# Kernel tuning notes

Measured on AMD Instinct MI355X. Metric: run time of the kernel, lower is better.

The kernel has to match this reference:

```python
import jax, jax.numpy as jnp
import numpy as np

D_MODEL = 1024
N_HEADS = 16
D_K = D_MODEL // N_HEADS
SIGMA = 1.0
NUM_ITERS = 3
PAD_POS = 10000.0


def setup_inputs() -> dict:
    rng = jax.random.key(0)
    ks = jax.random.split(rng, 16)
    B, Lq, Lk = 8, 512, 512
    s = 1.0 / np.sqrt(D_MODEL).astype(np.float32)
    return {
        "query": jax.random.normal(ks[0], (B, Lq, D_MODEL), jnp.float32),
        "key": jax.random.normal(ks[1], (B, Lk, D_MODEL), jnp.float32),
        "value": jax.random.normal(ks[2], (B, Lk, D_MODEL), jnp.float32),
        "query_lengths": jax.random.randint(ks[3], (B,), 2, Lq),
        "key_lengths": jax.random.randint(ks[4], (B,), 2, Lk),
        "Wq": jax.random.normal(ks[5], (D_MODEL, D_MODEL), jnp.float32) * s,
        "bq": jnp.zeros((D_MODEL,), jnp.float32),
        "Wk": jax.random.normal(ks[6], (D_MODEL, D_MODEL), jnp.float32) * s,
        "bk": jnp.zeros((D_MODEL,), jnp.float32),
        "Wv": jax.random.normal(ks[7], (D_MODEL, D_MODEL), jnp.float32) * s,
        "bv": jnp.zeros((D_MODEL,), jnp.float32),
        "Wo": jax.random.normal(ks[8], (D_MODEL, D_MODEL), jnp.float32) * s,
        "bo": jnp.zeros((D_MODEL,), jnp.float32),
        "pos_scale": jnp.ones((1,), jnp.float32),
        "pos_bias": jnp.zeros((1,), jnp.float32),
    }


def _init_positions(lengths, max_len, scale, bias):
    # vectorized tcr_pep init: linspace(-L/2, L/2, L) per row, pad -> 10000
    j = jnp.arange(max_len, dtype=jnp.float32)[None, :]          # [1, L]
    L = lengths.astype(jnp.float32)[:, None]                      # [B, 1]
    step = jnp.where(L > 1.0, L / (L - 1.0), 0.0)                 # linspace step
    pos = (-L / 2.0 + j * step) * scale + bias
    pad = jnp.arange(max_len)[None, :] >= lengths[:, None]
    return jnp.where(pad, PAD_POS, pos)


def _distance_attention(qp, kp):
    d2 = (qp[:, :, None] - kp[:, None, :]) ** 2                   # [B, Lq, Lk]
    attn = jnp.exp(-d2 / (2.0 * SIGMA * SIGMA))
    masked = (qp[:, :, None] >= 1000.0) | (kp[:, None, :] >= 1000.0)
    return jnp.where(masked, 0.0, attn)


def _update_positions(qp, kp, attn):
    qn = attn / jnp.clip(attn.sum(-1, keepdims=True), 1e-9)
    qp_new = jnp.einsum('bqk,bk->bq', qn, kp)
    at = attn.transpose(0, 2, 1)
    kn = at / jnp.clip(at.sum(-1, keepdims=True), 1e-9)
    kp_new = jnp.einsum('bkq,bq->bk', kn, qp)
    qp_new = jnp.where(qp >= 1000.0, PAD_POS, qp_new)
    kp_new = jnp.where(kp >= 1000.0, PAD_POS, kp_new)
    return qp_new, kp_new


def reference(query, key, value, query_lengths, key_lengths,
              Wq, bq, Wk, bk, Wv, bv, Wo, bo, pos_scale, pos_bias):
    B, Lq, _ = query.shape
    Lk = key.shape[1]

    def split_heads(x):
        return x.reshape(B, -1, N_HEADS, D_K).transpose(0, 2, 1, 3)  # [B,H,L,Dk]

    q = split_heads(query @ Wq.T + bq)
    k = split_heads(key @ Wk.T + bk)
    v = split_heads(value @ Wv.T + bv)

    qp = _init_positions(query_lengths, Lq, pos_scale, pos_bias)  # [B, Lq]
    kp = _init_positions(key_lengths, Lk, pos_scale, pos_bias)    # [B, Lk]

    scores = jnp.einsum('bhqd,bhkd->bhqk', q, k) / jnp.sqrt(jnp.float32(D_K))
    attn = jax.nn.softmax(scores, axis=-1)                        # [B,H,Lq,Lk]

    for _ in range(NUM_ITERS):
        da = _distance_attention(qp, kp)                          # [B,Lq,Lk]
        comb = attn * da[:, None, :, :]
        comb = comb / jnp.clip(comb.sum(-1, keepdims=True), 1e-9)
        qp, kp = _update_positions(qp, kp, da)
        attn = comb

    ctx = jnp.einsum('bhqk,bhkd->bhqd', attn, v)
    ctx = ctx.transpose(0, 2, 1, 3).reshape(B, Lq, D_MODEL)
    out = ctx @ Wo.T + bo
    return out, attn.mean(axis=1)
```

## Files before the change

kernel.cpp:

```cpp
#include <hip/hip_runtime.h>
#include <math.h>

#define B_  8
#define LQ  512
#define LK  512
#define DM  1024
#define NH  16
#define DK  64
constexpr float PADP = 10000.0f;

typedef short s16x8 __attribute__((ext_vector_type(8)));
typedef float f32x4 __attribute__((ext_vector_type(4)));

__device__ inline unsigned short f2b1(float f) {
    unsigned u = __float_as_uint(f);
    unsigned r = (u + 0x7fffu + ((u >> 16) & 1u)) >> 16;
    return (unsigned short)r;
}
__device__ inline float b2f1(unsigned short h) {
    return __uint_as_float(((unsigned)h) << 16);
}

__global__ __launch_bounds__(256) void f2b_all_kernel(
    const float* __restrict__ query, const float* __restrict__ key,
    const float* __restrict__ value,
    const float* __restrict__ Wq, const float* __restrict__ Wk,
    const float* __restrict__ Wv, const float* __restrict__ Wo,
    unsigned short* __restrict__ xq, unsigned short* __restrict__ xk,
    unsigned short* __restrict__ xv,
    unsigned short* __restrict__ wqb, unsigned short* __restrict__ wkb,
    unsigned short* __restrict__ wvb, unsigned short* __restrict__ wob)
{
    const int s = blockIdx.y;
    const float* src;
    unsigned short* dst;
    if (s < 4)       { src = query + ((size_t)s << 20);       dst = xq + ((size_t)s << 20); }
    else if (s < 8)  { src = key   + ((size_t)(s - 4) << 20); dst = xk + ((size_t)(s - 4) << 20); }
    else if (s < 12) { src = value + ((size_t)(s - 8) << 20); dst = xv + ((size_t)(s - 8) << 20); }
    else {
        const int w = s - 12;
        src = (w == 0) ? Wq : (w == 1) ? Wk : (w == 2) ? Wv : Wo;
        dst = (w == 0) ? wqb : (w == 1) ? wkb : (w == 2) ? wvb : wob;
    }
    const int i = blockIdx.x * 256 + threadIdx.x;
    const float4 v = *(const float4*)&src[(size_t)i * 4];
    ushort4 o;
    o.x = f2b1(v.x); o.y = f2b1(v.y); o.z = f2b1(v.z); o.w = f2b1(v.w);
    *(ushort4*)&dst[(size_t)i * 4] = o;
}

template <int PHASE>
__global__ __launch_bounds__(512) void daRow_kernel(
    const int* __restrict__ qlen, const int* __restrict__ klen,
    const float* __restrict__ pscale, const float* __restrict__ pbias,
    float* __restrict__ posQ,
    const float* __restrict__ posKin, float* __restrict__ posKout,
    const float* __restrict__ rsIn, const float* __restrict__ rdIn,
    const float* __restrict__ colSIn, const float* __restrict__ colDIn,
    float* __restrict__ rsOut, float* __restrict__ rdOut,
    float* __restrict__ colSOut, float* __restrict__ colDOut,
    unsigned short* __restrict__ Dplane)
{
    constexpr int NCH = 16, QC = LQ / NCH;
    __shared__ float kpl[LK];
    __shared__ float csp[8][LK], cdp[8][LK];
    const int chunk = blockIdx.x, b = blockIdx.y;
    const int t = threadIdx.x, w = t >> 6, lane = t & 63;

    float scale = 0.0f, bias = 0.0f;
    if (PHASE == 0) { scale = pscale[0]; bias = pbias[0]; }

    if (PHASE == 0) {
        const int kl = klen[b];
        const float Lf = (float)kl;
        const float step = (Lf > 1.0f) ? Lf / (Lf - 1.0f) : 0.0f;
        const float pos = (-Lf * 0.5f + (float)t * step) * scale + bias;
        const float kv = (t >= kl) ? PADP : pos;
        kpl[t] = kv;
        if (chunk == 0) posKout[b * LK + t] = kv;
    } else {
        float colsum = 0.0f, coldot = 0.0f;
#pragma unroll
        for (int c = 0; c < NCH; ++c) {
            colsum += colSIn[((size_t)b * NCH + c) * LK + t];
            coldot += colDIn[((size_t)b * NCH + c) * LK + t];
        }
        const float prev = posKin[b * LK + t];
        const float kv = (prev >= 1000.0f) ? PADP : coldot / fmaxf(colsum, 1e-9f);
        kpl[t] = kv;
        if (PHASE == 1 && chunk == 0) posKout[b * LK + t] = kv;
    }
    __syncthreads();

    float cs[8] = {0,0,0,0,0,0,0,0}, cd[8] = {0,0,0,0,0,0,0,0};
    unsigned short* Dbb = Dplane + (size_t)b * LQ * LK;

    for (int qi = chunk * QC + w; qi < chunk * QC + QC; qi += 8) {
        float qpv;
        if (PHASE == 0) {
            const int ql = qlen[b];
            const float Lf = (float)ql;
            const float step = (Lf > 1.0f) ? Lf / (Lf - 1.0f) : 0.0f;
            qpv = (qi >= ql) ? PADP : (-Lf * 0.5f + (float)qi * step) * scale + bias;
            if (lane == 0) posQ[b * LQ + qi] = qpv;
        } else {
            const float prev = posQ[b * LQ + qi];
            qpv = (prev >= 1000.0f) ? PADP
                : rdIn[b * LQ + qi] / fmaxf(rsIn[b * LQ + qi], 1e-9f);
            if (PHASE == 1 && lane == 0) posQ[b * LQ + qi] = qpv;
        }
        const bool qpad = (qpv >= 1000.0f);
        float rsum = 0.0f, rdot = 0.0f;
#pragma unroll
        for (int c = 0; c < 8; ++c) {
            const int k = lane + 64 * c;
            const float kpv = kpl[k];
            const float d = qpv - kpv;
            float e = (qpad || (kpv >= 1000.0f)) ? 0.0f : __expf(-0.5f * d * d);
            if (PHASE < 2) { rsum += e; rdot += e * kpv; cs[c] += e; cd[c] += e * qpv; }
            Dbb[(size_t)qi * LK + k] = f2b1(e);
        }
        if (PHASE < 2) {
#pragma unroll
            for (int o = 32; o > 0; o >>= 1) {
                rsum += __shfl_xor(rsum, o);
                rdot += __shfl_xor(rdot, o);
            }
            if (lane == 0) { rsOut[b * LQ + qi] = rsum; rdOut[b * LQ + qi] = rdot; }
        }
    }
    if (PHASE < 2) {
#pragma unroll
        for (int c = 0; c < 8; ++c) {
            csp[w][lane + 64 * c] = cs[c];
            cdp[w][lane + 64 * c] = cd[c];
        }
        __syncthreads();
        float s = 0.0f, dd = 0.0f;
        for (int ww = 0; ww < 8; ++ww) { s += csp[ww][t]; dd += cdp[ww][t]; }
        colSOut[((size_t)b * NCH + chunk) * LK + t] = s;
        colDOut[((size_t)b * NCH + chunk) * LK + t] = dd;
    }
}

__global__ __launch_bounds__(256) void transpose_bf16(
    const unsigned short* __restrict__ in, unsigned short* __restrict__ out,
    int Mn, int Nn)
{
    __shared__ unsigned short tile[64][65];
    const int m0 = blockIdx.y * 64, n0 = blockIdx.x * 64;
    const int t = threadIdx.x;
    const int r = t >> 3, c8 = (t & 7) * 8;
#pragma unroll
    for (int rr = 0; rr < 64; rr += 32) {
        const uint4 v = *(const uint4*)&in[(size_t)(m0 + r + rr) * Nn + n0 + c8];
        const unsigned short* pv = (const unsigned short*)&v;
#pragma unroll
        for (int j = 0; j < 8; ++j) tile[r + rr][c8 + j] = pv[j];
    }
    __syncthreads();
#pragma unroll
    for (int rr = 0; rr < 64; rr += 32) {
        unsigned short tmp[8];
#pragma unroll
        for (int j = 0; j < 8; ++j) tmp[j] = tile[c8 + j][r + rr];
        *(uint4*)&out[(size_t)(n0 + r + rr) * Mn + m0 + c8] = *(uint4*)tmp;
    }
}

template <bool OB>
__global__ __launch_bounds__(256) void gemm_bf16_nt(
    const unsigned short* __restrict__ A,
    const unsigned short* __restrict__ Bt,
    void* __restrict__ Cv,
    const float* __restrict__ bias,
    int M, int N, int K)
{
    constexpr int BKP = 40;
    __shared__ short As[64 * BKP];
    __shared__ short Bs[128 * BKP];
    const int m0 = blockIdx.y * 64, n0 = blockIdx.x * 128;
    const int t = threadIdx.x;
    const int wid = t >> 6, lane = t & 63;
    const int wr = wid >> 1, wc = wid & 1;
    const int lr = lane & 15, lk = (lane >> 4) * 8;

    f32x4 acc[2][4] = {};

    const int arow = t >> 2, aseg = (t & 3) * 8;
    const int brow = t >> 1, bseg = (t & 1) * 16;

    for (int kb = 0; kb < K; kb += 32) {
        const uint4 av  = *(const uint4*)&A[(size_t)(m0 + arow) * K + kb + aseg];
        const uint4 bv0 = *(const uint4*)&Bt[(size_t)(n0 + brow) * K + kb + bseg];
        const uint4 bv1 = *(const uint4*)&Bt[(size_t)(n0 + brow) * K + kb + bseg + 8];
        __syncthreads();
        *(uint4*)&As[arow * BKP + aseg] = av;
        *(uint4*)&Bs[brow * BKP + bseg] = bv0;
        *(uint4*)&Bs[brow * BKP + bseg + 8] = bv1;
        __syncthreads();

        s16x8 af[2], bf[4];
#pragma unroll
        for (int i = 0; i < 2; ++i)
            af[i] = *(const s16x8*)&As[(wr * 32 + i * 16 + lr) * BKP + lk];
#pragma unroll
        for (int j = 0; j < 4; ++j)
            bf[j] = *(const s16x8*)&Bs[(wc * 64 + j * 16 + lr) * BKP + lk];
#pragma unroll
        for (int i = 0; i < 2; ++i)
#pragma unroll
            for (int j = 0; j < 4; ++j)
                acc[i][j] = __builtin_amdgcn_mfma_f32_16x16x32_bf16(
                    af[i], bf[j], acc[i][j], 0, 0, 0);
    }

    const int r0 = (lane >> 4) * 4;
#pragma unroll
    for (int i = 0; i < 2; ++i) {
        const int row = m0 + wr * 32 + i * 16 + r0;
#pragma unroll
        for (int j = 0; j < 4; ++j) {
            const int col = n0 + wc * 64 + j * 16 + lr;
            const float bvv = bias ? bias[col] : 0.0f;
#pragma unroll
            for (int r = 0; r < 4; ++r) {
                const float val = acc[i][j][r] + bvv;
                if (OB) ((unsigned short*)Cv)[(size_t)(row + r) * N + col] = f2b1(val);
                else    ((float*)Cv)[(size_t)(row + r) * N + col] = val;
            }
        }
    }
}

__global__ __launch_bounds__(256) void scores_mfma(
    const unsigned short* __restrict__ Qb,
    const unsigned short* __restrict__ Kb,
    float* __restrict__ S, int hbase)
{
    constexpr int BKP = 72;
    __shared__ short As[128 * BKP];
    __shared__ short Bs[128 * BKP];
    const int z = blockIdx.z;
    const int b = z >> 3, hh = z & 7;
    const int hcol = (hbase + hh) * DK;
    const int m0 = blockIdx.y * 128, n0 = blockIdx.x * 128;
    const int t = threadIdx.x;
    const int wid = t >> 6, lane = t & 63;
    const int wr = wid >> 1, wc = wid & 1;
    const int lr = lane & 15, lk = (lane >> 4) * 8;

    const int srow = t >> 1, sseg = (t & 1) * 32;
    {
        const unsigned short* ag = &Qb[((size_t)(b * LQ + m0 + srow)) * DM + hcol + sseg];
        const unsigned short* bg = &Kb[((size_t)(b * LK + n0 + srow)) * DM + hcol + sseg];
#pragma unroll
        for (int s = 0; s < 4; ++s) {
            *(uint4*)&As[srow * BKP + sseg + s * 8] = *(const uint4*)(ag + s * 8);
            *(uint4*)&Bs[srow * BKP + sseg + s * 8] = *(const uint4*)(bg + s * 8);
        }
    }
    __syncthreads();

    f32x4 acc[4][4] = {};
#pragma unroll
    for (int kh = 0; kh < 2; ++kh) {
        s16x8 af[4], bf[4];
#pragma unroll
        for (int i = 0; i < 4; ++i)
            af[i] = *(const s16x8*)&As[(wr * 64 + i * 16 + lr) * BKP + kh * 32 + lk];
#pragma unroll
        for (int j = 0; j < 4; ++j)
            bf[j] = *(const s16x8*)&Bs[(wc * 64 + j * 16 + lr) * BKP + kh * 32 + lk];
#pragma unroll
        for (int i = 0; i < 4; ++i)
#pragma unroll
            for (int j = 0; j < 4; ++j)
                acc[i][j] = __builtin_amdgcn_mfma_f32_16x16x32_bf16(
                    af[i], bf[j], acc[i][j], 0, 0, 0);
    }

    const int r0 = (lane >> 4) * 4;
#pragma unroll
    for (int i = 0; i < 4; ++i) {
        const int row = m0 + wr * 64 + i * 16 + r0;
#pragma unroll
        for (int j = 0; j < 4; ++j) {
            const int col = n0 + wc * 64 + j * 16 + lr;
#pragma unroll
            for (int r = 0; r < 4; ++r)
                S[((size_t)z * LQ + row + r) * LK + col] = acc[i][j][r] * 0.125f;
        }
    }
}

__global__ __launch_bounds__(256) void ctx_mfma(
    const unsigned short* __restrict__ Ab,
    const unsigned short* __restrict__ VbT,
    unsigned short* __restrict__ ctxb, int hbase)
{
    constexpr int BKP = 72;
    __shared__ short As[64 * BKP];
    __shared__ short Bs[64 * BKP];
    const int z = blockIdx.z;
    const int b = z >> 3, hh = z & 7;
    const int hcol = (hbase + hh) * DK;
    const int q0 = blockIdx.y * 64;
    const int t = threadIdx.x;
    const int wid = t >> 6, lane = t & 63;
    const int wr = wid >> 1, wc = wid & 1;
    const int lr = lane & 15, lk = (lane >> 4) * 8;

    const unsigned short* Abase = Ab + ((size_t)z * LQ + q0) * LK;
    const unsigned short* Bbase = VbT + (size_t)hcol * (B_ * LK) + (size_t)b * LK;

    f32x4 acc[2][2] = {};
    const int srow = t >> 2, sseg = (t & 3) * 16;

    for (int kb = 0; kb < LK; kb += 64) {
        const uint4 a0 = *(const uint4*)&Abase[(size_t)srow * LK + kb + sseg];
        const uint4 a1 = *(const uint4*)&Abase[(size_t)srow * LK + kb + sseg + 8];
        const uint4 b0 = *(const uint4*)&Bbase[(size_t)srow * (B_ * LK) + kb + sseg];
        const uint4 b1 = *(const uint4*)&Bbase[(size_t)srow * (B_ * LK) + kb + sseg + 8];
        __syncthreads();
        *(uint4*)&As[srow * BKP + sseg] = a0;
        *(uint4*)&As[srow * BKP + sseg + 8] = a1;
        *(uint4*)&Bs[srow * BKP + sseg] = b0;
        *(uint4*)&Bs[srow * BKP + sseg + 8] = b1;
        __syncthreads();

#pragma unroll
        for (int kh = 0; kh < 2; ++kh) {
            s16x8 af[2], bf[2];
#pragma unroll
            for (int i = 0; i < 2; ++i)
                af[i] = *(const s16x8*)&As[(wr * 32 + i * 16 + lr) * BKP + kh * 32 + lk];
#pragma unroll
            for (int j = 0; j < 2; ++j)
                bf[j] = *(const s16x8*)&Bs[(wc * 32 + j * 16 + lr) * BKP + kh * 32 + lk];
#pragma unroll
            for (int i = 0; i < 2; ++i)
#pragma unroll
                for (int j = 0; j < 2; ++j)
                    acc[i][j] = __builtin_amdgcn_mfma_f32_16x16x32_bf16(
                        af[i], bf[j], acc[i][j], 0, 0, 0);
        }
    }

    const int r0 = (lane >> 4) * 4;
#pragma unroll
    for (int i = 0; i < 2; ++i) {
        const int row = b * LQ + q0 + wr * 32 + i * 16 + r0;
#pragma unroll
        for (int j = 0; j < 2; ++j) {
            const int col = hcol + wc * 32 + j * 16 + lr;
#pragma unroll
            for (int r = 0; r < 4; ++r)
                ctxb[(size_t)(row + r) * DM + col] = f2b1(acc[i][j][r]);
        }
    }
}

template <bool BT>
__global__ __launch_bounds__(256) void gemm64(
    const float* __restrict__ A, int lda, long aS1, long aS2,
    const float* __restrict__ Bm, int ldb, long bS1, long bS2,
    float* __restrict__ C, int ldc, long cS1, long cS2,
    const float* __restrict__ bias, int K, float alpha, int zshift)
{
    const int z = blockIdx.z;
    const long z1 = z >> zshift;
    const long z2 = z & ((1 << zshift) - 1);
    A  += z1 * aS1 + z2 * aS2;
    Bm += z1 * bS1 + z2 * bS2;
    C  += z1 * cS1 + z2 * cS2;

    const int m0 = blockIdx.y * 64, n0 = blockIdx.x * 64;
    __shared__ float As[32][68];
    __shared__ float Bs[32][68];
    const int t = threadIdx.x;
    const int ty = t >> 4, tx = t & 15;

    float acc[4][4];
#pragma unroll
    for (int i = 0; i < 4; ++i)
#pragma unroll
        for (int j = 0; j < 4; ++j) acc[i][j] = 0.0f;

    const int mA = t >> 3;
    const int kA = (t & 7) * 4;

    for (int kb = 0; kb < K; kb += 32) {
        {
            const float4 a0 = *(const float4*)&A[(size_t)(m0 + mA) * lda + kb + kA];
            const float4 a1 = *(const float4*)&A[(size_t)(m0 + mA + 32) * lda + kb + kA];
            As[kA + 0][mA] = a0.x; As[kA + 1][mA] = a0.y; As[kA + 2][mA] = a0.z; As[kA + 3][mA] = a0.w;
            As[kA + 0][mA + 32] = a1.x; As[kA + 1][mA + 32] = a1.y; As[kA + 2][mA + 32] = a1.z; As[kA + 3][mA + 32] = a1.w;
        }
        if (BT) {
            const float4 b0 = *(const float4*)&Bm[(size_t)(n0 + mA) * ldb + kb + kA];
            const float4 b1 = *(const float4*)&Bm[(size_t)(n0 + mA + 32) * ldb + kb + kA];
            Bs[kA + 0][mA] = b0.x; Bs[kA + 1][mA] = b0.y; Bs[kA + 2][mA] = b0.z; Bs[kA + 3][mA] = b0.w;
            Bs[kA + 0][mA + 32] = b1.x; Bs[kA + 1][mA + 32] = b1.y; Bs[kA + 2][mA + 32] = b1.z; Bs[kA + 3][mA + 32] = b1.w;
        } else {
            const int kB = t >> 4;
            const int nB = (t & 15) * 4;
            const float4 b0 = *(const float4*)&Bm[(size_t)(kb + kB) * ldb + n0 + nB];
            const float4 b1 = *(const float4*)&Bm[(size_t)(kb + kB + 16) * ldb + n0 + nB];
            *(float4*)&Bs[kB][nB] = b0;
            *(float4*)&Bs[kB + 16][nB] = b1;
        }
        __syncthreads();

#pragma unroll
        for (int kk = 0; kk < 32; ++kk) {
            const float4 av = *(const float4*)&As[kk][ty * 4];
            const float4 bv = *(const float4*)&Bs[kk][tx * 4];
            const float a[4] = {av.x, av.y, av.z, av.w};
            const float bb[4] = {bv.x, bv.y, bv.z, bv.w};
#pragma unroll
            for (int i = 0; i < 4; ++i)
#pragma unroll
                for (int j = 0; j < 4; ++j)
                    acc[i][j] = fmaf(a[i], bb[j], acc[i][j]);
        }
        __syncthreads();
    }

#pragma unroll
    for (int i = 0; i < 4; ++i) {
        const int row = m0 + ty * 4 + i;
        float4 o;
        o.x = acc[i][0] * alpha;
        o.y = acc[i][1] * alpha;
        o.z = acc[i][2] * alpha;
        o.w = acc[i][3] * alpha;
        if (bias) {
            o.x += bias[n0 + tx * 4 + 0];
            o.y += bias[n0 + tx * 4 + 1];
            o.z += bias[n0 + tx * 4 + 2];
            o.w += bias[n0 + tx * 4 + 3];
        }
        *(float4*)&C[(size_t)row * ldc + n0 + tx * 4] = o;
    }
}

template <bool BF16OUT>
__global__ __launch_bounds__(256) void softmaxP_kernel(
    float* __restrict__ S, const unsigned short* __restrict__ D,
    void* __restrict__ AOut, float* __restrict__ meanOut,
    int nheads, int accumulate)
{
    const int b = blockIdx.x >> 9, q = blockIdx.x & 511;
    const int t = threadIdx.x, w = t >> 6, lane = t & 63;
    __shared__ float Pl[3][LK];
    __shared__ float part[4][LK];
    const size_t NPB = (size_t)B_ * LQ * LK;
    const size_t rowoff = ((size_t)b * LQ + q) * LK;

    for (int i = t; i < LK; i += 256) {
        Pl[0][i] = b2f1(D[rowoff + i]);
        Pl[1][i] = b2f1(D[NPB + rowoff + i]);
        Pl[2][i] = b2f1(D[2 * NPB + rowoff + i]);
    }
    __syncthreads();

    float macc[8];
#pragma unroll
    for (int j = 0; j < 8; ++j) macc[j] = 0.0f;

    for (int h = w; h < nheads; h += 4) {
        const size_t roff = (((size_t)b * nheads + h) * LQ + q) * LK;
        const float* row = S + roff;
        float v[8];
        const float4 s0 = *(const float4*)&row[lane * 8];
        const float4 s1 = *(const float4*)&row[lane * 8 + 4];
        v[0] = s0.x; v[1] = s0.y; v[2] = s0.z; v[3] = s0.w;
        v[4] = s1.x; v[5] = s1.y; v[6] = s1.z; v[7] = s1.w;
        float mx = v[0];
#pragma unroll
        for (int j = 1; j < 8; ++j) mx = fmaxf(mx, v[j]);
#pragma unroll
        for (int o = 32; o > 0; o >>= 1) mx = fmaxf(mx, __shfl_xor(mx, o));
        float zz = 0.0f;
#pragma unroll
        for (int j = 0; j < 8; ++j) { v[j] = __expf(v[j] - mx); zz += v[j]; }
#pragma unroll
        for (int o = 32; o > 0; o >>= 1) zz += __shfl_xor(zz, o);
        const float invz = 1.0f / zz;
#pragma unroll
        for (int j = 0; j < 8; ++j) v[j] *= invz;

#pragma unroll
        for (int it = 0; it < 3; ++it) {
            float s = 0.0f;
#pragma unroll
            for (int j = 0; j < 8; ++j) {
                v[j] *= Pl[it][lane * 8 + j];
                s += v[j];
            }
#pragma unroll
            for (int o = 32; o > 0; o >>= 1) s += __shfl_xor(s, o);
            const float inv = 1.0f / fmaxf(s, 1e-9f);
#pragma unroll
            for (int j = 0; j < 8; ++j) v[j] *= inv;
        }

#pragma unroll
        for (int j = 0; j < 8; ++j) macc[j] += v[j];

        if (BF16OUT) {
            unsigned short* arow = (unsigned short*)AOut + roff;
            ushort4 u0, u1;
            u0.x = f2b1(v[0]); u0.y = f2b1(v[1]); u0.z = f2b1(v[2]); u0.w = f2b1(v[3]);
            u1.x = f2b1(v[4]); u1.y = f2b1(v[5]); u1.z = f2b1(v[6]); u1.w = f2b1(v[7]);
            *(ushort4*)&arow[lane * 8] = u0;
            *(ushort4*)&arow[lane * 8 + 4] = u1;
        } else {
            float* arow = (float*)AOut + roff;
            *(float4*)&arow[lane * 8] = make_float4(v[0], v[1], v[2], v[3]);
            *(float4*)&arow[lane * 8 + 4] = make_float4(v[4], v[5], v[6], v[7]);
        }
    }

    *(float4*)&part[w][lane * 8] = make_float4(macc[0], macc[1], macc[2], macc[3]);
    *(float4*)&part[w][lane * 8 + 4] = make_float4(macc[4], macc[5], macc[6], macc[7]);
    __syncthreads();

    for (int i = t; i < LK; i += 256) {
        const float m = (part[0][i] + part[1][i] + part[2][i] + part[3][i]) * (1.0f / 16.0f);
        const size_t oi = ((size_t)b * LQ + q) * LK + i;
        meanOut[oi] = accumulate ? (meanOut[oi] + m) : m;
    }
}

extern "C" void kernel_launch(void* const* d_in, const int* in_sizes, int n_in,
                              void* d_out, int out_size, void* d_ws, size_t ws_size,
                              hipStream_t stream)
{
    const float* query  = (const float*)d_in[0];
    const float* key    = (const float*)d_in[1];
    const float* value  = (const float*)d_in[2];
    const int*   qlen   = (const int*)d_in[3];
    const int*   klen   = (const int*)d_in[4];
    const float* Wq     = (const float*)d_in[5];
    const float* bq     = (const float*)d_in[6];
    const float* Wk     = (const float*)d_in[7];
    const float* bk     = (const float*)d_in[8];
    const float* Wv     = (const float*)d_in[9];
    const float* bv     = (const float*)d_in[10];
    const float* Wo     = (const float*)d_in[11];
    const float* bo     = (const float*)d_in[12];
    const float* pscale = (const float*)d_in[13];
    const float* pbias  = (const float*)d_in[14];

    float* out     = (float*)d_out;
    float* meanOut = out + (size_t)B_ * LQ * DM;

    const size_t NQKV = (size_t)B_ * LQ * DM;
    const size_t NP   = (size_t)B_ * LQ * LK;
    const size_t NW   = (size_t)DM * DM;
    const size_t NSg  = (size_t)B_ * 8 * LQ * LK;
    const size_t NPOS = (size_t)B_ * LQ;
    const size_t NCOL = (size_t)B_ * 16 * LK;

    unsigned short* Dbuf = (unsigned short*)d_ws;
    float* posQ  = (float*)(Dbuf + 3 * NP);
    float* posK1 = posQ + NPOS;
    float* posK2 = posK1 + NPOS;
    float* rs1   = posK2 + NPOS;
    float* rd1   = rs1 + NPOS;
    float* rs2   = rd1 + NPOS;
    float* rd2   = rs2 + NPOS;
    float* colS1 = rd2 + NPOS;
    float* colD1 = colS1 + NCOL;
    float* colS2 = colD1 + NCOL;
    float* colD2 = colS2 + NCOL;
    float* fend  = colD2 + NCOL;
    unsigned short* Qb   = (unsigned short*)fend;
    unsigned short* Kb   = Qb + NQKV;
    unsigned short* Vb   = Kb + NQKV;
    unsigned short* VbT  = Vb + NQKV;
    unsigned short* ctxb = VbT + NQKV;
    unsigned short* wqb  = ctxb + NQKV;
    unsigned short* wkb  = wqb + NW;
    unsigned short* wvb  = wkb + NW;
    unsigned short* wob  = wvb + NW;
    unsigned short* Ab   = wob + NW;
    float* Sg = (float*)(Ab + NSg);
    unsigned short* xq = Ab;
    unsigned short* xk = xq + NQKV;
    unsigned short* xv = xk + NQKV;

    const size_t need_full = (size_t)((char*)(Sg + NSg) - (char*)d_ws);

    if (ws_size >= need_full) {
        dim3 gDa(16, B_);
        daRow_kernel<0><<<gDa, 512, 0, stream>>>(qlen, klen, pscale, pbias,
            posQ, nullptr, posK1,
            nullptr, nullptr, nullptr, nullptr,
            rs1, rd1, colS1, colD1, Dbuf);
        daRow_kernel<1><<<gDa, 512, 0, stream>>>(qlen, klen, pscale, pbias,
            posQ, posK1, posK2,
            rs1, rd1, colS1, colD1,
            rs2, rd2, colS2, colD2, Dbuf + NP);
        daRow_kernel<2><<<gDa, 512, 0, stream>>>(qlen, klen, pscale, pbias,
            posQ, posK2, nullptr,
            rs2, rd2, colS2, colD2,
            nullptr, nullptr, nullptr, nullptr, Dbuf + 2 * NP);

        dim3 gF(1024, 16);
        f2b_all_kernel<<<gF, 256, 0, stream>>>(query, key, value, Wq, Wk, Wv, Wo,
                                               xq, xk, xv, wqb, wkb, wvb, wob);

        dim3 gP(DM / 128, (B_ * LQ) / 64);
        gemm_bf16_nt<true><<<gP, 256, 0, stream>>>(xq, wqb, Qb, bq, B_ * LQ, DM, DM);
        gemm_bf16_nt<true><<<gP, 256, 0, stream>>>(xk, wkb, Kb, bk, B_ * LQ, DM, DM);
        gemm_bf16_nt<true><<<gP, 256, 0, stream>>>(xv, wvb, Vb, bv, B_ * LQ, DM, DM);

        dim3 gT(DM / 64, (B_ * LK) / 64);
        transpose_bf16<<<gT, 256, 0, stream>>>(Vb, VbT, B_ * LK, DM);

        for (int g = 0; g < 2; ++g) {
            dim3 gS(LK / 128, LQ / 128, B_ * 8);
            scores_mfma<<<gS, 256, 0, stream>>>(Qb, Kb, Sg, g * 8);
            softmaxP_kernel<true><<<B_ * LQ, 256, 0, stream>>>(Sg, Dbuf, Ab, meanOut, 8, g);
            dim3 gC(1, LQ / 64, B_ * 8);
            ctx_mfma<<<gC, 256, 0, stream>>>(Ab, VbT, ctxb, g * 8);
        }

        gemm_bf16_nt<false><<<gP, 256, 0, stream>>>(ctxb, wob, out, bo, B_ * LQ, DM, DM);
        return;
    }

    float* qbuf = (float*)d_ws;
    float* kbuf = qbuf + NQKV;
    float* vbuf = kbuf + NQKV;
    unsigned short* Dfb = (unsigned short*)(vbuf + NQKV);
    float* Sfb  = (float*)(Dfb + 3 * NP);
    float* ctxbuf = Sfb + NP;
    float* pQ  = ctxbuf + NQKV;
    float* pK1 = pQ + NPOS;
    float* pK2 = pK1 + NPOS;
    float* frs1 = pK2 + NPOS;
    float* frd1 = frs1 + NPOS;
    float* frs2 = frd1 + NPOS;
    float* frd2 = frs2 + NPOS;
    float* fcS1 = frd2 + NPOS;
    float* fcD1 = fcS1 + NCOL;
    float* fcS2 = fcD1 + NCOL;
    float* fcD2 = fcS2 + NCOL;

    dim3 gDa(16, B_);
    daRow_kernel<0><<<gDa, 512, 0, stream>>>(qlen, klen, pscale, pbias,
        pQ, nullptr, pK1, nullptr, nullptr, nullptr, nullptr,
        frs1, frd1, fcS1, fcD1, Dfb);
    daRow_kernel<1><<<gDa, 512, 0, stream>>>(qlen, klen, pscale, pbias,
        pQ, pK1, pK2, frs1, frd1, fcS1, fcD1,
        frs2, frd2, fcS2, fcD2, Dfb + NP);
    daRow_kernel<2><<<gDa, 512, 0, stream>>>(qlen, klen, pscale, pbias,
        pQ, pK2, nullptr, frs2, frd2, fcS2, fcD2,
        nullptr, nullptr, nullptr, nullptr, Dfb + 2 * NP);

    dim3 gProj(DM / 64, (B_ * LQ) / 64, 1);
    gemm64<true><<<gProj, 256, 0, stream>>>(query, DM, 0, 0, Wq, DM, 0, 0,
                                            qbuf, DM, 0, 0, bq, DM, 1.0f, 0);
    gemm64<true><<<gProj, 256, 0, stream>>>(key, DM, 0, 0, Wk, DM, 0, 0,
                                            kbuf, DM, 0, 0, bk, DM, 1.0f, 0);
    gemm64<true><<<gProj, 256, 0, stream>>>(value, DM, 0, 0, Wv, DM, 0, 0,
                                            vbuf, DM, 0, 0, bv, DM, 1.0f, 0);
    for (int h = 0; h < NH; ++h) {
        dim3 gS2(LK / 64, LQ / 64, B_);
        gemm64<true><<<gS2, 256, 0, stream>>>(
            qbuf + h * DK, DM, (long)LQ * DM, 0,
            kbuf + h * DK, DM, (long)LK * DM, 0,
            Sfb, LK, (long)LQ * LK, 0,
            nullptr, DK, 0.125f, 0);
        softmaxP_kernel<false><<<B_ * LQ, 256, 0, stream>>>(Sfb, Dfb, Sfb, meanOut, 1, h > 0 ? 1 : 0);
        dim3 gC2(1, LQ / 64, B_);
        gemm64<false><<<gC2, 256, 0, stream>>>(
            Sfb, LK, (long)LQ * LK, 0,
            vbuf + h * DK, DM, (long)LK * DM, 0,
            ctxbuf + h * DK, DM, (long)LQ * DM, 0,
            nullptr, LK, 1.0f, 0);
    }
    dim3 gO(DM / 64, (B_ * LQ) / 64, 1);
    gemm64<true><<<gO, 256, 0, stream>>>(ctxbuf, DM, 0, 0, Wo, DM, 0, 0,
                                         out, DM, 0, 0, bo, DM, 1.0f, 0);
}
```

Baseline: 232.8 us.

## Fuse score GEMM, softmax and distance reweighting into one attention kernel

Replaces the two-pass scores_mfma + softmaxP pipeline with a single kernel per (batch, head, 64-query tile). It computes QK^T with MFMA, performs the softmax and the three distance-attention reweight/normalize iterations in registers, and writes bf16 probabilities directly. This removes the fp32 score buffer round trip through global memory and the per-group kernel launches. The head-mean is moved to a separate kernel that reads the bf16 probabilities. The fused kernel uses 512 threads with large register accumulators and several block-wide reductions, which may limit occupancy. The head-mean is now computed from bf16-rounded values.

```diff
diff --git a/kernel.cpp b/kernel.cpp
--- a/kernel.cpp
+++ b/kernel.cpp
@@ -233,78 +233,234 @@
     }
 }
 
-__global__ __launch_bounds__(256) void scores_mfma(
+template <bool ISMAX>
+__device__ inline void rowreduce(float v[4][4], float (*red)[64],
+                                 int wid, int lr, int rbase)
+{
+#pragma unroll
+    for (int i = 0; i < 4; ++i)
+#pragma unroll
+        for (int r = 0; r < 4; ++r) {
+            float x = v[i][r];
+#pragma unroll
+            for (int o = 1; o < 16; o <<= 1) {
+                const float y = __shfl_xor(x, o);
+                x = ISMAX ? fmaxf(x, y) : (x + y);
+            }
+            v[i][r] = x;
+        }
+    __syncthreads();
+    if (lr == 0) {
+#pragma unroll
+        for (int i = 0; i < 4; ++i)
+#pragma unroll
+            for (int r = 0; r < 4; ++r)
+                red[wid][i * 16 + rbase + r] = v[i][r];
+    }
+    __syncthreads();
+#pragma unroll
+    for (int i = 0; i < 4; ++i)
+#pragma unroll
+        for (int r = 0; r < 4; ++r) {
+            float x = red[0][i * 16 + rbase + r];
+#pragma unroll
+            for (int ww = 1; ww < 8; ++ww) {
+                const float y = red[ww][i * 16 + rbase + r];
+                x = ISMAX ? fmaxf(x, y) : (x + y);
+            }
+            v[i][r] = x;
+        }
+}
+
+__global__ __launch_bounds__(512) void attn_fused(
     const unsigned short* __restrict__ Qb,
     const unsigned short* __restrict__ Kb,
-    float* __restrict__ S, int hbase)
-{
-    constexpr int BKP = 72;
-    __shared__ short As[128 * BKP];
-    __shared__ short Bs[128 * BKP];
-    const int z = blockIdx.z;
-    const int b = z >> 3, hh = z & 7;
-    const int hcol = (hbase + hh) * DK;
-    const int m0 = blockIdx.y * 128, n0 = blockIdx.x * 128;
+    const unsigned short* __restrict__ D,
+    unsigned short* __restrict__ Ab)
+{
+    constexpr int KP = 72;
+    constexpr int PP = 264;
+    __shared__ short pool[23040];
+    __shared__ float red[8][64];
+    short* Qs = pool;
+    short* Ks = pool + 4608;
+    short* Ps = pool + 4608;
+
+    const int z = blockIdx.y;
+    const int b = z >> 4, h = z & 15;
+    const int q0 = blockIdx.x * 64;
     const int t = threadIdx.x;
     const int wid = t >> 6, lane = t & 63;
-    const int wr = wid >> 1, wc = wid & 1;
-    const int lr = lane & 15, lk = (lane >> 4) * 8;
-
-    const int srow = t >> 1, sseg = (t & 1) * 32;
+    const int lr = lane & 15, lkq = (lane >> 4) * 8;
+    const int rbase = (lane >> 4) * 4;
+
     {
-        const unsigned short* ag = &Qb[((size_t)(b * LQ + m0 + srow)) * DM + hcol + sseg];
-        const unsigned short* bg = &Kb[((size_t)(b * LK + n0 + srow)) * DM + hcol + sseg];
-#pragma unroll
-        for (int s = 0; s < 4; ++s) {
-            *(uint4*)&As[srow * BKP + sseg + s * 8] = *(const uint4*)(ag + s * 8);
-            *(uint4*)&Bs[srow * BKP + sseg + s * 8] = *(const uint4*)(bg + s * 8);
-        }
-    }
-    __syncthreads();
-
-    f32x4 acc[4][4] = {};
-#pragma unroll
+        const int row = t >> 3, seg = (t & 7) * 8;
+        *(uint4*)&Qs[row * KP + seg] =
+            *(const uint4*)&Qb[((size_t)(b * LQ + q0 + row)) * DM + h * DK + seg];
+    }
+
+    f32x4 acc[2][4][2] = {};
+
     for (int kh = 0; kh < 2; ++kh) {
-        s16x8 af[4], bf[4];
+        __syncthreads();
+        {
+            const int row = t >> 1, seg = (t & 1) * 32;
+            const unsigned short* src =
+                &Kb[((size_t)(b * LK + kh * 256 + row)) * DM + h * DK + seg];
+#pragma unroll
+            for (int s = 0; s < 4; ++s)
+                *(uint4*)&Ks[row * KP + seg + s * 8] = *(const uint4*)(src + s * 8);
+        }
+        __syncthreads();
+
+#pragma unroll
+        for (int ks = 0; ks < 2; ++ks) {
+            s16x8 af[4], bf[2];
+#pragma unroll
+            for (int i = 0; i < 4; ++i)
+                af[i] = *(const s16x8*)&Qs[(i * 16 + lr) * KP + ks * 32 + lkq];
+#pragma unroll
+            for (int j = 0; j < 2; ++j)
+                bf[j] = *(const s16x8*)&Ks[(wid * 32 + j * 16 + lr) * KP + ks * 32 + lkq];
+#pragma unroll
+            for (int i = 0; i < 4; ++i)
+#pragma unroll
+                for (int j = 0; j < 2; ++j)
+                    acc[kh][i][j] = __builtin_amdgcn_mfma_f32_16x16x32_bf16(
+                        af[i], bf[j], acc[kh][i][j], 0, 0, 0);
+        }
+    }
+
+    float M[4][4];
+#pragma unroll
+    for (int i = 0; i < 4; ++i)
+#pragma unroll
+        for (int r = 0; r < 4; ++r) {
+            float m = acc[0][i][0][r];
+            m = fmaxf(m, acc[0][i][1][r]);
+            m = fmaxf(m, acc[1][i][0][r]);
+            m = fmaxf(m, acc[1][i][1][r]);
+            M[i][r] = m;
+        }
+    rowreduce<true>(M, red, wid, lr, rbase);
+
+    float S[4][4] = {};
+#pragma unroll
+    for (int kh = 0; kh < 2; ++kh)
 #pragma unroll
         for (int i = 0; i < 4; ++i)
-            af[i] = *(const s16x8*)&As[(wr * 64 + i * 16 + lr) * BKP + kh * 32 + lk];
-#pragma unroll
-        for (int j = 0; j < 4; ++j)
-            bf[j] = *(const s16x8*)&Bs[(wc * 64 + j * 16 + lr) * BKP + kh * 32 + lk];
+#pragma unroll
+            for (int j = 0; j < 2; ++j)
+#pragma unroll
+                for (int r = 0; r < 4; ++r) {
+                    const float e = __expf((acc[kh][i][j][r] - M[i][r]) * 0.125f);
+                    acc[kh][i][j][r] = e;
+                    S[i][r] += e;
+                }
+    rowreduce<false>(S, red, wid, lr, rbase);
+#pragma unroll
+    for (int i = 0; i < 4; ++i)
+#pragma unroll
+        for (int r = 0; r < 4; ++r) S[i][r] = 1.0f / S[i][r];
+#pragma unroll
+    for (int kh = 0; kh < 2; ++kh)
 #pragma unroll
         for (int i = 0; i < 4; ++i)
 #pragma unroll
-            for (int j = 0; j < 4; ++j)
-                acc[i][j] = __builtin_amdgcn_mfma_f32_16x16x32_bf16(
-                    af[i], bf[j], acc[i][j], 0, 0, 0);
-    }
-
-    const int r0 = (lane >> 4) * 4;
-#pragma unroll
-    for (int i = 0; i < 4; ++i) {
-        const int row = m0 + wr * 64 + i * 16 + r0;
-#pragma unroll
-        for (int j = 0; j < 4; ++j) {
-            const int col = n0 + wc * 64 + j * 16 + lr;
-#pragma unroll
-            for (int r = 0; r < 4; ++r)
-                S[((size_t)z * LQ + row + r) * LK + col] = acc[i][j][r] * 0.125f;
-        }
-    }
+            for (int j = 0; j < 2; ++j)
+#pragma unroll
+                for (int r = 0; r < 4; ++r)
+                    acc[kh][i][j][r] *= S[i][r];
+
+    for (int it = 0; it < 3; ++it) {
+        float T[4][4] = {};
+        for (int kh = 0; kh < 2; ++kh) {
+            __syncthreads();
+            {
+                const int row = t >> 3, seg = (t & 7) * 32;
+                const unsigned short* src =
+                    &D[(((size_t)it * B_ + b) * LQ + q0 + row) * LK + kh * 256 + seg];
+#pragma unroll
+                for (int s = 0; s < 4; ++s)
+                    *(uint4*)&Ps[row * PP + seg + s * 8] = *(const uint4*)(src + s * 8);
+            }
+            __syncthreads();
+#pragma unroll
+            for (int i = 0; i < 4; ++i)
+#pragma unroll
+                for (int j = 0; j < 2; ++j) {
+                    const int col = wid * 32 + j * 16 + lr;
+#pragma unroll
+                    for (int r = 0; r < 4; ++r) {
+                        const int row = i * 16 + rbase + r;
+                        const float p = b2f1(Ps[row * PP + col]);
+                        acc[kh][i][j][r] *= p;
+                        T[i][r] += acc[kh][i][j][r];
+                    }
+                }
+        }
+        rowreduce<false>(T, red, wid, lr, rbase);
+#pragma unroll
+        for (int i = 0; i < 4; ++i)
+#pragma unroll
+            for (int r = 0; r < 4; ++r) T[i][r] = 1.0f / fmaxf(T[i][r], 1e-9f);
+#pragma unroll
+        for (int kh = 0; kh < 2; ++kh)
+#pragma unroll
+            for (int i = 0; i < 4; ++i)
+#pragma unroll
+                for (int j = 0; j < 2; ++j)
+#pragma unroll
+                    for (int r = 0; r < 4; ++r)
+                        acc[kh][i][j][r] *= T[i][r];
+    }
+
+#pragma unroll
+    for (int kh = 0; kh < 2; ++kh)
+#pragma unroll
+        for (int i = 0; i < 4; ++i)
+#pragma unroll
+            for (int j = 0; j < 2; ++j) {
+                const int col = kh * 256 + wid * 32 + j * 16 + lr;
+#pragma unroll
+                for (int r = 0; r < 4; ++r) {
+                    const int row = i * 16 + rbase + r;
+                    Ab[((size_t)z * LQ + q0 + row) * LK + col] = f2b1(acc[kh][i][j][r]);
+                }
+            }
+}
+
+__global__ __launch_bounds__(256) void meanB_kernel(
+    const unsigned short* __restrict__ Ab, float* __restrict__ meanOut)
+{
+    const int b = blockIdx.x >> 9, q = blockIdx.x & 511;
+    const int t = threadIdx.x;
+    const int c0 = t * 2;
+    float s0 = 0.0f, s1 = 0.0f;
+#pragma unroll
+    for (int h = 0; h < 16; ++h) {
+        const unsigned short* row = Ab + (((size_t)(b * 16 + h)) * LQ + q) * LK;
+        const unsigned v = *(const unsigned*)&row[c0];
+        s0 += b2f1((unsigned short)(v & 0xffff));
+        s1 += b2f1((unsigned short)(v >> 16));
+    }
+    float* o = meanOut + ((size_t)b * LQ + q) * LK + c0;
+    o[0] = s0 * (1.0f / 16.0f);
+    o[1] = s1 * (1.0f / 16.0f);
 }
 
 __global__ __launch_bounds__(256) void ctx_mfma(
     const unsigned short* __restrict__ Ab,
     const unsigned short* __restrict__ VbT,
-    unsigned short* __restrict__ ctxb, int hbase)
+    unsigned short* __restrict__ ctxb)
 {
     constexpr int BKP = 72;
     __shared__ short As[64 * BKP];
     __shared__ short Bs[64 * BKP];
     const int z = blockIdx.z;
-    const int b = z >> 3, hh = z & 7;
-    const int hcol = (hbase + hh) * DK;
+    const int b = z >> 4, h = z & 15;
+    const int hcol = h * DK;
     const int q0 = blockIdx.y * 64;
     const int t = threadIdx.x;
     const int wid = t >> 6, lane = t & 63;
@@ -560,7 +716,7 @@
     const size_t NQKV = (size_t)B_ * LQ * DM;
     const size_t NP   = (size_t)B_ * LQ * LK;
     const size_t NW   = (size_t)DM * DM;
-    const size_t NSg  = (size_t)B_ * 8 * LQ * LK;
+    const size_t NS   = (size_t)B_ * NH * LQ * LK;
     const size_t NPOS = (size_t)B_ * LQ;
     const size_t NCOL = (size_t)B_ * 16 * LK;
 
@@ -587,12 +743,11 @@
     unsigned short* wvb  = wkb + NW;
     unsigned short* wob  = wvb + NW;
     unsigned short* Ab   = wob + NW;
-    float* Sg = (float*)(Ab + NSg);
     unsigned short* xq = Ab;
     unsigned short* xk = xq + NQKV;
     unsigned short* xv = xk + NQKV;
 
-    const size_t need_full = (size_t)((char*)(Sg + NSg) - (char*)d_ws);
+    const size_t need_full = (size_t)((char*)(Ab + NS) - (char*)d_ws);
 
     if (ws_size >= need_full) {
         dim3 gDa(16, B_);
@@ -621,13 +776,13 @@
         dim3 gT(DM / 64, (B_ * LK) / 64);
         transpose_bf16<<<gT, 256, 0, stream>>>(Vb, VbT, B_ * LK, DM);
 
-        for (int g = 0; g < 2; ++g) {
-            dim3 gS(LK / 128, LQ / 128, B_ * 8);
-            scores_mfma<<<gS, 256, 0, stream>>>(Qb, Kb, Sg, g * 8);
-            softmaxP_kernel<true><<<B_ * LQ, 256, 0, stream>>>(Sg, Dbuf, Ab, meanOut, 8, g);
-            dim3 gC(1, LQ / 64, B_ * 8);
-            ctx_mfma<<<gC, 256, 0, stream>>>(Ab, VbT, ctxb, g * 8);
-        }
+        dim3 gA(LQ / 64, B_ * NH);
+        attn_fused<<<gA, 512, 0, stream>>>(Qb, Kb, Dbuf, Ab);
+
+        meanB_kernel<<<B_ * LQ, 256, 0, stream>>>(Ab, meanOut);
+
+        dim3 gC(1, LQ / 64, B_ * NH);
+        ctx_mfma<<<gC, 256, 0, stream>>>(Ab, VbT, ctxb);
 
         gemm_bf16_nt<false><<<gP, 256, 0, stream>>>(ctxb, wob, out, bo, B_ * LQ, DM, DM);
         return;
```

After: 273.6 us. +17.5%, slower.
